# Optimization experiments

Hardware: AMD Instinct MI355X
Metric: run time of the kernel (lower is better)

The kernel has to match this reference:

```python
import jax, jax.numpy as jnp
import numpy as np

MODES, WIDTH, DEPTH, IN_F, OUT_F, HID = 8, 16, 3, 1, 1, 64


def setup_inputs() -> dict:
    key = jax.random.key(0)
    ks = jax.random.split(key, 12)
    B, H, W = 8, 512, 512
    scale = 1.0 / (WIDTH * WIDTH)
    inp = {
        'x': jax.random.normal(ks[0], (B, IN_F, H, W), dtype=jnp.float32),
        'fc0_w': jax.random.normal(ks[1], (IN_F, WIDTH), dtype=jnp.float32) * 0.5,
        'fc0_b': jax.random.normal(ks[2], (WIDTH,), dtype=jnp.float32) * 0.1,
        # complex spectral weights stored as real/imag parts, stacked over depth
        'spec_wr': jax.random.normal(ks[3], (DEPTH, WIDTH, WIDTH, MODES, MODES), dtype=jnp.float32) * scale,
        'spec_wi': jax.random.normal(ks[4], (DEPTH, WIDTH, WIDTH, MODES, MODES), dtype=jnp.float32) * scale,
        # 1x1 convs as [depth, out, in] matmuls + bias
        'conv_w': jax.random.normal(ks[5], (DEPTH, WIDTH, WIDTH), dtype=jnp.float32) * 0.25,
        'conv_b': jax.random.normal(ks[6], (DEPTH, WIDTH), dtype=jnp.float32) * 0.1,
        'fc1_w': jax.random.normal(ks[7], (WIDTH, HID), dtype=jnp.float32) * 0.25,
        'fc1_b': jax.random.normal(ks[8], (HID,), dtype=jnp.float32) * 0.1,
        'fc2_w': jax.random.normal(ks[9], (HID, OUT_F), dtype=jnp.float32) * 0.125,
        'fc2_b': jax.random.normal(ks[10], (OUT_F,), dtype=jnp.float32) * 0.1,
    }
    return inp


def _spectral_conv(x, w):
    # x: [B, Ci, H, W] real; w: [Ci, Co, m, m] complex
    B, C, H, W = x.shape
    m = w.shape[2]
    x_ft = jnp.fft.rfft2(x, norm='forward')  # [B, Ci, H, W//2+1]
    out_modes = jnp.einsum('bixy,ioxy->boxy', x_ft[:, :, :m, :m], w)
    out_ft = jnp.zeros((B, w.shape[1], H, W // 2 + 1), dtype=out_modes.dtype)
    out_ft = out_ft.at[:, :, :m, :m].set(out_modes)
    return jnp.fft.irfft2(out_ft, s=(H, W), norm='forward')


def reference(x, fc0_w, fc0_b, spec_wr, spec_wi, conv_w, conv_b, fc1_w, fc1_b, fc2_w, fc2_b):
    # lift: [B,C,H,W] -> channels-last linear -> [B,width,H,W]
    h = jnp.einsum('bchw,cd->bdhw', x, fc0_w) + fc0_b[None, :, None, None]
    for d in range(DEPTH):
        w_c = (spec_wr[d] + 1j * spec_wi[d]).astype(jnp.complex64)
        y = _spectral_conv(h, w_c)
        local = jnp.einsum('bchw,oc->bohw', h, conv_w[d]) + conv_b[d][None, :, None, None]
        h = y + local
    h = jnp.einsum('bchw,cd->bdhw', h, fc1_w) + fc1_b[None, :, None, None]
    h = jax.nn.relu(h)
    out = jnp.einsum('bchw,cd->bdhw', h, fc2_w) + fc2_b[None, :, None, None]
    return out
```

## Files before the change

### kernel.cpp

```cpp
#include <hip/hip_runtime.h>
#include <math.h>

#define NB 8
#define NH 512
#define NW 512
#define ANG512 0.01227184630308513f
#define SPEC_D 16384

typedef __attribute__((ext_vector_type(8))) _Float16 f16x8;
typedef __attribute__((ext_vector_type(4))) float    f32x4;

__global__ __launch_bounds__(256) void k_pre(const float* __restrict__ x,
                                             float* __restrict__ P) {
    __shared__ float wred[8][16];
    const int tid = threadIdx.x;
    const int w = tid >> 6, lane = tid & 63;
    const int gid = blockIdx.x;
    const int b = gid >> 6, rg = gid & 63;

    #pragma unroll
    for (int rr = 0; rr < 2; ++rr) {
        const int row = rg * 8 + w + 4 * rr;
        const float* xr = x + ((size_t)(b * NH + row)) * NW;

        float p[16];
        #pragma unroll
        for (int j = 0; j < 16; ++j) p[j] = 0.f;

        #pragma unroll
        for (int j = 0; j < 4; ++j) {
            const int ww = lane + (j << 6);
            const float xa = xr[ww], xb = xr[ww + 256];
            const float a = xa + xb, d = xa - xb;
            float c1, s1;
            __sincosf(ANG512 * (float)ww, &s1, &c1);
            p[0] += a;
            p[1] = fmaf(d, c1, p[1]);
            p[9] = fmaf(-d, s1, p[9]);
            const float c2k = 2.f * c1;
            float ckm = 1.f, skm = 0.f, ck = c1, sk = s1;
            #pragma unroll
            for (int k = 2; k < 8; ++k) {
                const float cn = fmaf(c2k, ck, -ckm);
                const float sn = fmaf(c2k, sk, -skm);
                ckm = ck; skm = sk; ck = cn; sk = sn;
                const float v = (k & 1) ? d : a;
                p[k]     = fmaf(v, ck, p[k]);
                p[8 + k] = fmaf(-v, sk, p[8 + k]);
            }
        }
        #pragma unroll
        for (int m = 1; m < 64; m <<= 1) {
            #pragma unroll
            for (int j = 0; j < 16; ++j) p[j] += __shfl_xor(p[j], m);
        }
        if (lane < 16) wred[w + 4 * rr][lane] = p[lane];
    }
    __syncthreads();

    if (tid < 128) {
        const int kx = tid >> 4, q = tid & 15, qm = q & 7;
        float acc = 0.f;
        #pragma unroll
        for (int r = 0; r < 8; ++r) {
            const int row = rg * 8 + r;
            const int m = (kx * row) & 511;
            float cm, s2;
            __sincosf(ANG512 * (float)m, &s2, &cm);
            const float rre = wred[r][qm], rim = wred[r][8 + qm];
            acc += (q < 8) ? (rre * cm + rim * s2)
                           : (rim * cm - rre * s2);
        }
        P[((size_t)((b * 64 + rg) * 8 + kx)) * 16 + q] = acc;
    }
}

__global__ __launch_bounds__(256) void k_modes(
        const float* __restrict__ P,
        const float* __restrict__ spec_wr, const float* __restrict__ spec_wi,
        const float* __restrict__ conv_w, const float* __restrict__ conv_b,
        const float* __restrict__ fc0_w, const float* __restrict__ fc0_b,
        const float* __restrict__ fc1_w, const float* __restrict__ fc1_b,
        float* __restrict__ AH, float* __restrict__ gv, float* __restrict__ Kv) {
    __shared__ __align__(16) float sm[2640];
    float* red2  = sm;
    float* X2    = sm + 256;
    float* Xr    = sm + 272;
    float* Xi    = sm + 400;
    float* Fr    = sm + 528;
    float* Fi    = sm + 656;
    float* Ar    = sm + 784;
    float* Ai    = sm + 912;
    float* Pm    = sm + 1040;
    float* fc1_s = sm + 1552;
    float* ps    = sm + 2576;

    const int tid = threadIdx.x;
    const int bid = blockIdx.x;
    const int b = bid >> 3;
    const int kx = bid & 7;

    {
        const int o = tid >> 4, c = tid & 15;
        float s = 0.f;
        for (int k = 0; k < 16; ++k)
            s += conv_w[512 + o * 16 + k] * conv_w[256 + k * 16 + c];
        Pm[tid] = s;
    }
    Pm[256 + tid] = conv_w[512 + tid];
    #pragma unroll
    for (int k = 0; k < 4; ++k) fc1_s[tid + k * 256] = fc1_w[tid + k * 256];

    {
        const int q = tid & 15, c = tid >> 4;
        float acc = 0.f;
        #pragma unroll
        for (int m = 0; m < 4; ++m) {
            const int rg = c + 16 * m;
            acc += P[((size_t)((b * 64 + rg) * 8 + kx)) * 16 + q];
        }
        red2[c * 16 + q] = acc;
    }
    __syncthreads();
    if (tid < 16) {
        float s = 0.f;
        #pragma unroll
        for (int c = 0; c < 16; ++c) s += red2[c * 16 + tid];
        X2[tid] = s;
    }
    __syncthreads();

    const bool act = (tid < 128);
    const int o = tid >> 3, ky = tid & 7;
    if (act) {
        const float inv = 1.f / (512.f * 512.f);
        float xr0 = fc0_w[o] * X2[ky] * inv;
        float xi0 = fc0_w[o] * X2[8 + ky] * inv;
        if (kx == 0 && ky == 0) xr0 += fc0_b[o];
        Xr[o * 8 + ky] = xr0; Xi[o * 8 + ky] = xi0;
        Ar[o * 8 + ky] = 0.f; Ai[o * 8 + ky] = 0.f;
    }
    __syncthreads();

    for (int dd = 0; dd < 3; ++dd) {
        if (act) {
            float fr = 0.f, fi = 0.f;
            const float* wrp = spec_wr + (size_t)dd * SPEC_D + o * 64 + kx * 8 + ky;
            const float* wip = spec_wi + (size_t)dd * SPEC_D + o * 64 + kx * 8 + ky;
            #pragma unroll
            for (int i = 0; i < 16; ++i) {
                const float wre = wrp[i * 1024];
                const float wim = wip[i * 1024];
                const float xr0 = Xr[i * 8 + ky], xi0 = Xi[i * 8 + ky];
                fr += xr0 * wre - xi0 * wim;
                fi += xr0 * wim + xi0 * wre;
            }
            Fr[o * 8 + ky] = fr; Fi[o * 8 + ky] = fi;
        }
        __syncthreads();
        float xnr = 0.f, xni = 0.f;
        if (act) {
            float ar, ai;
            if (dd == 2) {
                ar = Fr[o * 8 + ky]; ai = Fi[o * 8 + ky];
            } else {
                ar = 0.f; ai = 0.f;
                #pragma unroll
                for (int c = 0; c < 16; ++c) {
                    const float pv = Pm[dd * 256 + o * 16 + c];
                    ar = fmaf(pv, Fr[c * 8 + ky], ar);
                    ai = fmaf(pv, Fi[c * 8 + ky], ai);
                }
            }
            Ar[o * 8 + ky] += ar; Ai[o * 8 + ky] += ai;
            if (dd < 2) {
                const float fr0 = Fr[o * 8 + ky], fi0 = Fi[o * 8 + ky];
                if (ky == 0) {
                    if (kx == 0) { xnr = fr0; xni = 0.f; }
                    else         { xnr = 0.5f * fr0; xni = 0.5f * fi0; }
                } else { xnr = fr0; xni = fi0; }
                #pragma unroll
                for (int c = 0; c < 16; ++c) {
                    const float cc = conv_w[dd * 256 + o * 16 + c];
                    xnr = fmaf(cc, Xr[c * 8 + ky], xnr);
                    xni = fmaf(cc, Xi[c * 8 + ky], xni);
                }
                if (kx == 0 && ky == 0) xnr += conv_b[dd * 16 + o];
            }
        }
        __syncthreads();
        if (act && dd < 2) { Xr[o * 8 + ky] = xnr; Xi[o * 8 + ky] = xni; }
        __syncthreads();
    }

    #pragma unroll
    for (int k2 = 0; k2 < 2; ++k2) {
        const int idx = tid + k2 * 256;
        const int hd = idx >> 3, ky2 = idx & 7;
        float ar = 0.f, ai = 0.f;
        #pragma unroll
        for (int c = 0; c < 16; ++c) {
            const float f = fc1_s[c * 64 + hd];
            ar = fmaf(f, Ar[c * 8 + ky2], ar);
            ai = fmaf(f, Ai[c * 8 + ky2], ai);
        }
        const float ck = (ky2 == 0) ? 1.f : 2.f;
        const size_t off = ((((size_t)(b * 64 + hd)) * 8 + ky2) * 8 + kx) * 2;
        AH[off]     = ck * ar;
        AH[off + 1] = ck * ai;
    }

    if (kx == 0) {
        if (tid < 16) {
            float su = 0.f, sb = 0.f;
            for (int c = 0; c < 16; ++c) {
                su += conv_w[tid * 16 + c] * fc0_w[c];
                sb += conv_w[tid * 16 + c] * fc0_b[c];
            }
            ps[tid] = su; ps[16 + tid] = sb;
        }
        __syncthreads();
        if (tid < 16) {
            float dv = 0.f, ev = conv_b[32 + tid];
            for (int k = 0; k < 16; ++k) {
                dv += Pm[tid * 16 + k] * ps[k];
                ev += Pm[tid * 16 + k] * (ps[16 + k] + conv_b[k]);
                ev += conv_w[512 + tid * 16 + k] * conv_b[16 + k];
            }
            ps[32 + tid] = dv; ps[48 + tid] = ev;
        }
        __syncthreads();
        if (tid < 64) {
            float g = 0.f, K = fc1_b[tid];
            for (int c = 0; c < 16; ++c) {
                g = fmaf(fc1_w[c * 64 + tid], ps[32 + c], g);
                K = fmaf(fc1_w[c * 64 + tid], ps[48 + c], K);
            }
            gv[b * 64 + tid] = g;
            Kv[b * 64 + tid] = K;
        }
    }
}

__global__ __launch_bounds__(256, 4) void k_head(
        const float* __restrict__ x, const float* __restrict__ AH,
        const float* __restrict__ gv, const float* __restrict__ Kv,
        const float* __restrict__ fc2_w, const float* __restrict__ fc2_b,
        float* __restrict__ out) {
    __shared__ __align__(16) _Float16 Ef[2][512][8];
    __shared__ __align__(16) _Float16 Apk[4][4][64][8];

    const int tid  = threadIdx.x;
    const int lane = tid & 63;
    const int rl   = tid >> 6;
    const int b    = blockIdx.x >> 7;
    const int rp   = blockIdx.x & 127;
    const int row  = rp * 4 + rl;

    #pragma unroll
    for (int pxi = 0; pxi < 2; ++pxi) {
        const int px = tid + pxi * 256;
        float c1, s1;
        __sincosf(ANG512 * (float)px, &s1, &c1);
        float ck = 1.f, sk = 0.f;
        #pragma unroll
        for (int k = 0; k < 8; ++k) {
            Ef[0][px][k] = (_Float16)ck;
            Ef[1][px][k] = (_Float16)(-sk);
            const float cn = ck * c1 - sk * s1;
            const float sn = sk * c1 + ck * s1;
            ck = cn; sk = sn;
        }
    }

    float ghr[16], w2r[16];
    {
        const int lg = lane >> 4;
        #pragma unroll
        for (int t = 0; t < 4; ++t)
            #pragma unroll
            for (int v = 0; v < 4; ++v) {
                const int hd = t * 16 + lg * 4 + v;
                ghr[t * 4 + v] = gv[b * 64 + hd];
                w2r[t * 4 + v] = fc2_w[hd];
            }
    }

    {
        float c1, s1;
        __sincosf(ANG512 * (float)row, &s1, &c1);
        float ctr[8], str[8];
        ctr[0] = 1.f; str[0] = 0.f; ctr[1] = c1; str[1] = s1;
        const float c2k = 2.f * c1;
        #pragma unroll
        for (int k = 2; k < 8; ++k) {
            ctr[k] = fmaf(c2k, ctr[k - 1], -ctr[k - 2]);
            str[k] = fmaf(c2k, str[k - 1], -str[k - 2]);
        }
        #pragma unroll
        for (int j = 0; j < 8; ++j) {
            const int idx = lane + j * 64;
            const int hd = idx >> 3, ky = idx & 7;
            const float4* ap = (const float4*)(AH + ((size_t)(b * 64 + hd) * 8 + ky) * 16);
            const float4 a0 = ap[0], a1 = ap[1], a2 = ap[2], a3 = ap[3];
            float wr = a0.x, wi = a0.y;
            wr = fmaf(a0.z, ctr[1], wr); wr = fmaf(-a0.w, str[1], wr);
            wi = fmaf(a0.z, str[1], wi); wi = fmaf(a0.w, ctr[1], wi);
            wr = fmaf(a1.x, ctr[2], wr); wr = fmaf(-a1.y, str[2], wr);
            wi = fmaf(a1.x, str[2], wi); wi = fmaf(a1.y, ctr[2], wi);
            wr = fmaf(a1.z, ctr[3], wr); wr = fmaf(-a1.w, str[3], wr);
            wi = fmaf(a1.z, str[3], wi); wi = fmaf(a1.w, ctr[3], wi);
            wr = fmaf(a2.x, ctr[4], wr); wr = fmaf(-a2.y, str[4], wr);
            wi = fmaf(a2.x, str[4], wi); wi = fmaf(a2.y, ctr[4], wi);
            wr = fmaf(a2.z, ctr[5], wr); wr = fmaf(-a2.w, str[5], wr);
            wi = fmaf(a2.z, str[5], wi); wi = fmaf(a2.w, ctr[5], wi);
            wr = fmaf(a3.x, ctr[6], wr); wr = fmaf(-a3.y, str[6], wr);
            wi = fmaf(a3.x, str[6], wi); wi = fmaf(a3.y, ctr[6], wi);
            wr = fmaf(a3.z, ctr[7], wr); wr = fmaf(-a3.w, str[7], wr);
            wi = fmaf(a3.w, ctr[7], wi); wi = fmaf(a3.z, str[7], wi);
            if (ky == 0) wr += Kv[b * 64 + hd];
            const _Float16 hr  = (_Float16)wr;
            const _Float16 hi_ = (_Float16)wi;
            Apk[rl][0][hd][ky] = hr;
            Apk[rl][1][hd][ky] = hi_;
            Apk[rl][2][hd][ky] = (_Float16)(wr - (float)hr);
            Apk[rl][3][hd][ky] = (_Float16)(wi - (float)hi_);
        }
    }
    __syncthreads();

    f16x8 a1[4];
    {
        const int kb = lane >> 4, m = lane & 15;
        #pragma unroll
        for (int t = 0; t < 4; ++t)
            a1[t] = *(const f16x8*)&Apk[rl][kb][t * 16 + m][0];
    }

    const int eb = (lane >> 4) & 1, n = lane & 15;
    const float fc2b = fc2_b[0];
    const float* xrow = x + ((size_t)(b * NH + row)) * NW;
    float* orow = out + ((size_t)(b * NH + row)) * NW;

    f16x8 bn0 = *(const f16x8*)&Ef[eb][n][0];
    f16x8 bn1 = *(const f16x8*)&Ef[eb][16 + n][0];
    float xn0 = xrow[n];
    float xn1 = xrow[16 + n];

    #pragma unroll 2
    for (int it = 0; it < 16; ++it) {
        const f16x8 b0 = bn0, b1 = bn1;
        const float x0 = xn0, x1 = xn1;
        if (it < 15) {
            const int pb = (it + 1) * 32 + n;
            bn0 = *(const f16x8*)&Ef[eb][pb][0];
            bn1 = *(const f16x8*)&Ef[eb][pb + 16][0];
            xn0 = xrow[pb];
            xn1 = xrow[pb + 16];
        }
        f32x4 c0[4], c1[4];
        #pragma unroll
        for (int t = 0; t < 4; ++t) {
            c0[t] = (f32x4){0.f, 0.f, 0.f, 0.f};
            c1[t] = (f32x4){0.f, 0.f, 0.f, 0.f};
            c0[t] = __builtin_amdgcn_mfma_f32_16x16x32_f16(a1[t], b0, c0[t], 0, 0, 0);
            c1[t] = __builtin_amdgcn_mfma_f32_16x16x32_f16(a1[t], b1, c1[t], 0, 0, 0);
        }
        float p0[4] = {0.f, 0.f, 0.f, 0.f};
        float p1[4] = {0.f, 0.f, 0.f, 0.f};
        #pragma unroll
        for (int t = 0; t < 4; ++t)
            #pragma unroll
            for (int v = 0; v < 4; ++v) {
                float s0 = fmaf(ghr[t * 4 + v], x0, c0[t][v]);
                float s1 = fmaf(ghr[t * 4 + v], x1, c1[t][v]);
                s0 = fmaxf(s0, 0.f);
                s1 = fmaxf(s1, 0.f);
                p0[v] = fmaf(s0, w2r[t * 4 + v], p0[v]);
                p1[v] = fmaf(s1, w2r[t * 4 + v], p1[v]);
            }
        float v0 = (p0[0] + p0[1]) + (p0[2] + p0[3]);
        float v1 = (p1[0] + p1[1]) + (p1[2] + p1[3]);
        v0 += __shfl_xor(v0, 16);
        v1 += __shfl_xor(v1, 16);
        v0 += __shfl_xor(v0, 32);
        v1 += __shfl_xor(v1, 32);
        if (lane < 16) {
            orow[it * 32 + lane]      = v0 + fc2b;
            orow[it * 32 + 16 + lane] = v1 + fc2b;
        }
    }
}

extern "C" void kernel_launch(void* const* d_in, const int* in_sizes, int n_in,
                              void* d_out, int out_size, void* d_ws, size_t ws_size,
                              hipStream_t stream) {
    const float* x       = (const float*)d_in[0];
    const float* fc0_w   = (const float*)d_in[1];
    const float* fc0_b   = (const float*)d_in[2];
    const float* spec_wr = (const float*)d_in[3];
    const float* spec_wi = (const float*)d_in[4];
    const float* conv_w  = (const float*)d_in[5];
    const float* conv_b  = (const float*)d_in[6];
    const float* fc1_w   = (const float*)d_in[7];
    const float* fc1_b   = (const float*)d_in[8];
    const float* fc2_w   = (const float*)d_in[9];
    const float* fc2_b   = (const float*)d_in[10];
    float* outp = (float*)d_out;

    char* ws = (char*)d_ws;
    float* P  = (float*)ws;
    float* AH = (float*)(ws + 262144);
    float* gv = (float*)(ws + 524288);
    float* Kv = (float*)(ws + 526336);

    k_pre<<<512, 256, 0, stream>>>(x, P);
    k_modes<<<64, 256, 0, stream>>>(P, spec_wr, spec_wi, conv_w, conv_b,
                                    fc0_w, fc0_b, fc1_w, fc1_b, AH, gv, Kv);
    k_head<<<1024, 256, 0, stream>>>(x, AH, gv, Kv, fc2_w, fc2_b, outp);
}
```

Before: 116.2 us.

## Fuse modes kernel into head kernel with per-batch flag synchronization

Merges the small 64-block mode-mixing kernel into the 1024-block head kernel. The first 64 blocks do the mode work, publish AH/gv/Kv with atomic stores and raise a per-batch release flag. Every block builds its twiddle tables first, then spins on its batch's flag before reading those values. This removes one kernel launch and its serialization gap, and lets the head's table setup overlap the mode computation. In exchange it relies on the producer blocks being scheduled (deadlock risk if they are not resident), uses only relaxed loads on the consumer side, and adds spin-wait overhead.

```diff
diff --git a/kernel.cpp b/kernel.cpp
--- a/kernel.cpp
+++ b/kernel.cpp
@@ -7,8 +7,13 @@
 #define ANG512 0.01227184630308513f
 #define SPEC_D 16384
 
+#define DEV_SCOPE __HIP_MEMORY_SCOPE_AGENT
+
 typedef __attribute__((ext_vector_type(8))) _Float16 f16x8;
 typedef __attribute__((ext_vector_type(4))) float    f32x4;
+
+__device__ int g_flag[256];
+__device__ int g_done[256];
 
 __global__ __launch_bounds__(256) void k_pre(const float* __restrict__ x,
                                              float* __restrict__ P) {
@@ -75,177 +80,14 @@
     }
 }
 
-__global__ __launch_bounds__(256) void k_modes(
-        const float* __restrict__ P,
+__global__ __launch_bounds__(256, 4) void k_mh(
+        const float* __restrict__ x, const float* __restrict__ P,
         const float* __restrict__ spec_wr, const float* __restrict__ spec_wi,
         const float* __restrict__ conv_w, const float* __restrict__ conv_b,
         const float* __restrict__ fc0_w, const float* __restrict__ fc0_b,
         const float* __restrict__ fc1_w, const float* __restrict__ fc1_b,
-        float* __restrict__ AH, float* __restrict__ gv, float* __restrict__ Kv) {
-    __shared__ __align__(16) float sm[2640];
-    float* red2  = sm;
-    float* X2    = sm + 256;
-    float* Xr    = sm + 272;
-    float* Xi    = sm + 400;
-    float* Fr    = sm + 528;
-    float* Fi    = sm + 656;
-    float* Ar    = sm + 784;
-    float* Ai    = sm + 912;
-    float* Pm    = sm + 1040;
-    float* fc1_s = sm + 1552;
-    float* ps    = sm + 2576;
-
-    const int tid = threadIdx.x;
-    const int bid = blockIdx.x;
-    const int b = bid >> 3;
-    const int kx = bid & 7;
-
-    {
-        const int o = tid >> 4, c = tid & 15;
-        float s = 0.f;
-        for (int k = 0; k < 16; ++k)
-            s += conv_w[512 + o * 16 + k] * conv_w[256 + k * 16 + c];
-        Pm[tid] = s;
-    }
-    Pm[256 + tid] = conv_w[512 + tid];
-    #pragma unroll
-    for (int k = 0; k < 4; ++k) fc1_s[tid + k * 256] = fc1_w[tid + k * 256];
-
-    {
-        const int q = tid & 15, c = tid >> 4;
-        float acc = 0.f;
-        #pragma unroll
-        for (int m = 0; m < 4; ++m) {
-            const int rg = c + 16 * m;
-            acc += P[((size_t)((b * 64 + rg) * 8 + kx)) * 16 + q];
-        }
-        red2[c * 16 + q] = acc;
-    }
-    __syncthreads();
-    if (tid < 16) {
-        float s = 0.f;
-        #pragma unroll
-        for (int c = 0; c < 16; ++c) s += red2[c * 16 + tid];
-        X2[tid] = s;
-    }
-    __syncthreads();
-
-    const bool act = (tid < 128);
-    const int o = tid >> 3, ky = tid & 7;
-    if (act) {
-        const float inv = 1.f / (512.f * 512.f);
-        float xr0 = fc0_w[o] * X2[ky] * inv;
-        float xi0 = fc0_w[o] * X2[8 + ky] * inv;
-        if (kx == 0 && ky == 0) xr0 += fc0_b[o];
-        Xr[o * 8 + ky] = xr0; Xi[o * 8 + ky] = xi0;
-        Ar[o * 8 + ky] = 0.f; Ai[o * 8 + ky] = 0.f;
-    }
-    __syncthreads();
-
-    for (int dd = 0; dd < 3; ++dd) {
-        if (act) {
-            float fr = 0.f, fi = 0.f;
-            const float* wrp = spec_wr + (size_t)dd * SPEC_D + o * 64 + kx * 8 + ky;
-            const float* wip = spec_wi + (size_t)dd * SPEC_D + o * 64 + kx * 8 + ky;
-            #pragma unroll
-            for (int i = 0; i < 16; ++i) {
-                const float wre = wrp[i * 1024];
-                const float wim = wip[i * 1024];
-                const float xr0 = Xr[i * 8 + ky], xi0 = Xi[i * 8 + ky];
-                fr += xr0 * wre - xi0 * wim;
-                fi += xr0 * wim + xi0 * wre;
-            }
-            Fr[o * 8 + ky] = fr; Fi[o * 8 + ky] = fi;
-        }
-        __syncthreads();
-        float xnr = 0.f, xni = 0.f;
-        if (act) {
-            float ar, ai;
-            if (dd == 2) {
-                ar = Fr[o * 8 + ky]; ai = Fi[o * 8 + ky];
-            } else {
-                ar = 0.f; ai = 0.f;
-                #pragma unroll
-                for (int c = 0; c < 16; ++c) {
-                    const float pv = Pm[dd * 256 + o * 16 + c];
-                    ar = fmaf(pv, Fr[c * 8 + ky], ar);
-                    ai = fmaf(pv, Fi[c * 8 + ky], ai);
-                }
-            }
-            Ar[o * 8 + ky] += ar; Ai[o * 8 + ky] += ai;
-            if (dd < 2) {
-                const float fr0 = Fr[o * 8 + ky], fi0 = Fi[o * 8 + ky];
-                if (ky == 0) {
-                    if (kx == 0) { xnr = fr0; xni = 0.f; }
-                    else         { xnr = 0.5f * fr0; xni = 0.5f * fi0; }
-                } else { xnr = fr0; xni = fi0; }
-                #pragma unroll
-                for (int c = 0; c < 16; ++c) {
-                    const float cc = conv_w[dd * 256 + o * 16 + c];
-                    xnr = fmaf(cc, Xr[c * 8 + ky], xnr);
-                    xni = fmaf(cc, Xi[c * 8 + ky], xni);
-                }
-                if (kx == 0 && ky == 0) xnr += conv_b[dd * 16 + o];
-            }
-        }
-        __syncthreads();
-        if (act && dd < 2) { Xr[o * 8 + ky] = xnr; Xi[o * 8 + ky] = xni; }
-        __syncthreads();
-    }
-
-    #pragma unroll
-    for (int k2 = 0; k2 < 2; ++k2) {
-        const int idx = tid + k2 * 256;
-        const int hd = idx >> 3, ky2 = idx & 7;
-        float ar = 0.f, ai = 0.f;
-        #pragma unroll
-        for (int c = 0; c < 16; ++c) {
-            const float f = fc1_s[c * 64 + hd];
-            ar = fmaf(f, Ar[c * 8 + ky2], ar);
-            ai = fmaf(f, Ai[c * 8 + ky2], ai);
-        }
-        const float ck = (ky2 == 0) ? 1.f : 2.f;
-        const size_t off = ((((size_t)(b * 64 + hd)) * 8 + ky2) * 8 + kx) * 2;
-        AH[off]     = ck * ar;
-        AH[off + 1] = ck * ai;
-    }
-
-    if (kx == 0) {
-        if (tid < 16) {
-            float su = 0.f, sb = 0.f;
-            for (int c = 0; c < 16; ++c) {
-                su += conv_w[tid * 16 + c] * fc0_w[c];
-                sb += conv_w[tid * 16 + c] * fc0_b[c];
-            }
-            ps[tid] = su; ps[16 + tid] = sb;
-        }
-        __syncthreads();
-        if (tid < 16) {
-            float dv = 0.f, ev = conv_b[32 + tid];
-            for (int k = 0; k < 16; ++k) {
-                dv += Pm[tid * 16 + k] * ps[k];
-                ev += Pm[tid * 16 + k] * (ps[16 + k] + conv_b[k]);
-                ev += conv_w[512 + tid * 16 + k] * conv_b[16 + k];
-            }
-            ps[32 + tid] = dv; ps[48 + tid] = ev;
-        }
-        __syncthreads();
-        if (tid < 64) {
-            float g = 0.f, K = fc1_b[tid];
-            for (int c = 0; c < 16; ++c) {
-                g = fmaf(fc1_w[c * 64 + tid], ps[32 + c], g);
-                K = fmaf(fc1_w[c * 64 + tid], ps[48 + c], K);
-            }
-            gv[b * 64 + tid] = g;
-            Kv[b * 64 + tid] = K;
-        }
-    }
-}
-
-__global__ __launch_bounds__(256, 4) void k_head(
-        const float* __restrict__ x, const float* __restrict__ AH,
-        const float* __restrict__ gv, const float* __restrict__ Kv,
         const float* __restrict__ fc2_w, const float* __restrict__ fc2_b,
+        float* __restrict__ AH, float* __restrict__ gv, float* __restrict__ Kv,
         float* __restrict__ out) {
     __shared__ __align__(16) _Float16 Ef[2][512][8];
     __shared__ __align__(16) _Float16 Apk[4][4][64][8];
@@ -253,9 +95,172 @@
     const int tid  = threadIdx.x;
     const int lane = tid & 63;
     const int rl   = tid >> 6;
-    const int b    = blockIdx.x >> 7;
-    const int rp   = blockIdx.x & 127;
+    const int bid  = blockIdx.x;
+    const int cb   = bid >> 7;
+    const int rp   = bid & 127;
     const int row  = rp * 4 + rl;
+
+    if (bid < 64) {
+        float* psm   = (float*)&Apk[0][0][0][0];
+        float* red2  = psm;
+        float* X2    = psm + 256;
+        float* Xr    = psm + 272;
+        float* Xi    = psm + 400;
+        float* Fr    = psm + 528;
+        float* Fi    = psm + 656;
+        float* Ar    = psm + 784;
+        float* Ai    = psm + 912;
+        float* Pm    = psm + 1040;
+        float* fc1_s = psm + 1552;
+        float* ps    = psm + 2576;
+
+        const int b2 = bid >> 3;
+        const int kx = bid & 7;
+
+        {
+            const int o = tid >> 4, c = tid & 15;
+            float s = 0.f;
+            for (int k = 0; k < 16; ++k)
+                s += conv_w[512 + o * 16 + k] * conv_w[256 + k * 16 + c];
+            Pm[tid] = s;
+        }
+        Pm[256 + tid] = conv_w[512 + tid];
+        #pragma unroll
+        for (int k = 0; k < 4; ++k) fc1_s[tid + k * 256] = fc1_w[tid + k * 256];
+
+        {
+            const int q = tid & 15, c = tid >> 4;
+            float acc = 0.f;
+            #pragma unroll
+            for (int m = 0; m < 4; ++m) {
+                const int rg = c + 16 * m;
+                acc += P[((size_t)((b2 * 64 + rg) * 8 + kx)) * 16 + q];
+            }
+            red2[c * 16 + q] = acc;
+        }
+        __syncthreads();
+        if (tid < 16) {
+            float s = 0.f;
+            #pragma unroll
+            for (int c = 0; c < 16; ++c) s += red2[c * 16 + tid];
+            X2[tid] = s;
+        }
+        __syncthreads();
+
+        const bool act = (tid < 128);
+        const int o = tid >> 3, ky = tid & 7;
+        if (act) {
+            const float inv = 1.f / (512.f * 512.f);
+            float xr0 = fc0_w[o] * X2[ky] * inv;
+            float xi0 = fc0_w[o] * X2[8 + ky] * inv;
+            if (kx == 0 && ky == 0) xr0 += fc0_b[o];
+            Xr[o * 8 + ky] = xr0; Xi[o * 8 + ky] = xi0;
+            Ar[o * 8 + ky] = 0.f; Ai[o * 8 + ky] = 0.f;
+        }
+        __syncthreads();
+
+        for (int dd = 0; dd < 3; ++dd) {
+            if (act) {
+                float fr = 0.f, fi = 0.f;
+                const float* wrp = spec_wr + (size_t)dd * SPEC_D + o * 64 + kx * 8 + ky;
+                const float* wip = spec_wi + (size_t)dd * SPEC_D + o * 64 + kx * 8 + ky;
+                #pragma unroll
+                for (int i = 0; i < 16; ++i) {
+                    const float wre = wrp[i * 1024];
+                    const float wim = wip[i * 1024];
+                    const float xr0 = Xr[i * 8 + ky], xi0 = Xi[i * 8 + ky];
+                    fr += xr0 * wre - xi0 * wim;
+                    fi += xr0 * wim + xi0 * wre;
+                }
+                Fr[o * 8 + ky] = fr; Fi[o * 8 + ky] = fi;
+            }
+            __syncthreads();
+            float xnr = 0.f, xni = 0.f;
+            if (act) {
+                float ar, ai;
+                if (dd == 2) {
+                    ar = Fr[o * 8 + ky]; ai = Fi[o * 8 + ky];
+                } else {
+                    ar = 0.f; ai = 0.f;
+                    #pragma unroll
+                    for (int c = 0; c < 16; ++c) {
+                        const float pv = Pm[dd * 256 + o * 16 + c];
+                        ar = fmaf(pv, Fr[c * 8 + ky], ar);
+                        ai = fmaf(pv, Fi[c * 8 + ky], ai);
+                    }
+                }
+                Ar[o * 8 + ky] += ar; Ai[o * 8 + ky] += ai;
+                if (dd < 2) {
+                    const float fr0 = Fr[o * 8 + ky], fi0 = Fi[o * 8 + ky];
+                    if (ky == 0) {
+                        if (kx == 0) { xnr = fr0; xni = 0.f; }
+                        else         { xnr = 0.5f * fr0; xni = 0.5f * fi0; }
+                    } else { xnr = fr0; xni = fi0; }
+                    #pragma unroll
+                    for (int c = 0; c < 16; ++c) {
+                        const float cc = conv_w[dd * 256 + o * 16 + c];
+                        xnr = fmaf(cc, Xr[c * 8 + ky], xnr);
+                        xni = fmaf(cc, Xi[c * 8 + ky], xni);
+                    }
+                    if (kx == 0 && ky == 0) xnr += conv_b[dd * 16 + o];
+                }
+            }
+            __syncthreads();
+            if (act && dd < 2) { Xr[o * 8 + ky] = xnr; Xi[o * 8 + ky] = xni; }
+            __syncthreads();
+        }
+
+        #pragma unroll
+        for (int k2 = 0; k2 < 2; ++k2) {
+            const int idx = tid + k2 * 256;
+            const int hd = idx >> 3, ky2 = idx & 7;
+            float ar = 0.f, ai = 0.f;
+            #pragma unroll
+            for (int c = 0; c < 16; ++c) {
+                const float f = fc1_s[c * 64 + hd];
+                ar = fmaf(f, Ar[c * 8 + ky2], ar);
+                ai = fmaf(f, Ai[c * 8 + ky2], ai);
+            }
+            const float ck = (ky2 == 0) ? 1.f : 2.f;
+            const size_t off = ((((size_t)(b2 * 64 + hd)) * 8 + ky2) * 8 + kx) * 2;
+            __hip_atomic_store(&AH[off],     ck * ar, __ATOMIC_RELAXED, DEV_SCOPE);
+            __hip_atomic_store(&AH[off + 1], ck * ai, __ATOMIC_RELAXED, DEV_SCOPE);
+        }
+
+        if (kx == 0) {
+            if (tid < 16) {
+                float su = 0.f, sb = 0.f;
+                for (int c = 0; c < 16; ++c) {
+                    su += conv_w[tid * 16 + c] * fc0_w[c];
+                    sb += conv_w[tid * 16 + c] * fc0_b[c];
+                }
+                ps[tid] = su; ps[16 + tid] = sb;
+            }
+            __syncthreads();
+            if (tid < 16) {
+                float dv = 0.f, ev = conv_b[32 + tid];
+                for (int k = 0; k < 16; ++k) {
+                    dv += Pm[tid * 16 + k] * ps[k];
+                    ev += Pm[tid * 16 + k] * (ps[16 + k] + conv_b[k]);
+                    ev += conv_w[512 + tid * 16 + k] * conv_b[16 + k];
+                }
+                ps[32 + tid] = dv; ps[48 + tid] = ev;
+            }
+            __syncthreads();
+            if (tid < 64) {
+                float g = 0.f, K = fc1_b[tid];
+                for (int c = 0; c < 16; ++c) {
+                    g = fmaf(fc1_w[c * 64 + tid], ps[32 + c], g);
+                    K = fmaf(fc1_w[c * 64 + tid], ps[48 + c], K);
+                }
+                __hip_atomic_store(&gv[b2 * 64 + tid], g, __ATOMIC_RELAXED, DEV_SCOPE);
+                __hip_atomic_store(&Kv[b2 * 64 + tid], K, __ATOMIC_RELAXED, DEV_SCOPE);
+            }
+        }
+        __syncthreads();
+        if (tid == 0)
+            __hip_atomic_fetch_add(&g_flag[b2 * 32], 1, __ATOMIC_RELEASE, DEV_SCOPE);
+    }
 
     #pragma unroll
     for (int pxi = 0; pxi < 2; ++pxi) {
@@ -273,6 +278,18 @@
         }
     }
 
+    if (tid == 0) {
+        while (__hip_atomic_load(&g_flag[cb * 32], __ATOMIC_RELAXED, DEV_SCOPE) < 8)
+            __builtin_amdgcn_s_sleep(4);
+        const int d = __hip_atomic_fetch_add(&g_done[cb * 32], 1,
+                                             __ATOMIC_RELAXED, DEV_SCOPE);
+        if (d == 127) {
+            __hip_atomic_store(&g_flag[cb * 32], 0, __ATOMIC_RELAXED, DEV_SCOPE);
+            __hip_atomic_store(&g_done[cb * 32], 0, __ATOMIC_RELAXED, DEV_SCOPE);
+        }
+    }
+    __syncthreads();
+
     float ghr[16], w2r[16];
     {
         const int lg = lane >> 4;
@@ -281,7 +298,7 @@
             #pragma unroll
             for (int v = 0; v < 4; ++v) {
                 const int hd = t * 16 + lg * 4 + v;
-                ghr[t * 4 + v] = gv[b * 64 + hd];
+                ghr[t * 4 + v] = gv[cb * 64 + hd];
                 w2r[t * 4 + v] = fc2_w[hd];
             }
     }
@@ -301,7 +318,7 @@
         for (int j = 0; j < 8; ++j) {
             const int idx = lane + j * 64;
             const int hd = idx >> 3, ky = idx & 7;
-            const float4* ap = (const float4*)(AH + ((size_t)(b * 64 + hd) * 8 + ky) * 16);
+            const float4* ap = (const float4*)(AH + ((size_t)(cb * 64 + hd) * 8 + ky) * 16);
             const float4 a0 = ap[0], a1 = ap[1], a2 = ap[2], a3 = ap[3];
             float wr = a0.x, wi = a0.y;
             wr = fmaf(a0.z, ctr[1], wr); wr = fmaf(-a0.w, str[1], wr);
@@ -318,7 +335,7 @@
             wi = fmaf(a3.x, str[6], wi); wi = fmaf(a3.y, ctr[6], wi);
             wr = fmaf(a3.z, ctr[7], wr); wr = fmaf(-a3.w, str[7], wr);
             wi = fmaf(a3.w, ctr[7], wi); wi = fmaf(a3.z, str[7], wi);
-            if (ky == 0) wr += Kv[b * 64 + hd];
+            if (ky == 0) wr += Kv[cb * 64 + hd];
             const _Float16 hr  = (_Float16)wr;
             const _Float16 hi_ = (_Float16)wi;
             Apk[rl][0][hd][ky] = hr;
@@ -339,8 +356,8 @@
 
     const int eb = (lane >> 4) & 1, n = lane & 15;
     const float fc2b = fc2_b[0];
-    const float* xrow = x + ((size_t)(b * NH + row)) * NW;
-    float* orow = out + ((size_t)(b * NH + row)) * NW;
+    const float* xrow = x + ((size_t)(cb * NH + row)) * NW;
+    float* orow = out + ((size_t)(cb * NH + row)) * NW;
 
     f16x8 bn0 = *(const f16x8*)&Ef[eb][n][0];
     f16x8 bn1 = *(const f16x8*)&Ef[eb][16 + n][0];
@@ -415,7 +432,7 @@
     float* Kv = (float*)(ws + 526336);
 
     k_pre<<<512, 256, 0, stream>>>(x, P);
-    k_modes<<<64, 256, 0, stream>>>(P, spec_wr, spec_wi, conv_w, conv_b,
-                                    fc0_w, fc0_b, fc1_w, fc1_b, AH, gv, Kv);
-    k_head<<<1024, 256, 0, stream>>>(x, AH, gv, Kv, fc2_w, fc2_b, outp);
+    k_mh<<<1024, 256, 0, stream>>>(x, P, spec_wr, spec_wi, conv_w, conv_b,
+                                   fc0_w, fc0_b, fc1_w, fc1_b, fc2_w, fc2_b,
+                                   AH, gv, Kv, outp);
 }
```

New measurement: 119.3 us. +2.6%, slower.

## Split k_head work across more blocks with two waves per row

Applied to the files above, without the earlier changes.

Each k_head block now covers two rows and half the columns instead of four full rows. Two waves share one row: they split the AH twiddle packing work and each handles a quarter of the columns. This gives four times as many blocks, a smaller LDS footprint and a higher occupancy target, aimed at better latency hiding and load balance across CUs. In exchange, the sincos tables and the per-row AH packing are recomputed by more blocks, adding redundant setup work per output.

```diff
diff --git a/kernel.cpp b/kernel.cpp
--- a/kernel.cpp
+++ b/kernel.cpp
@@ -242,31 +242,35 @@
     }
 }
 
-__global__ __launch_bounds__(256, 4) void k_head(
+__global__ __launch_bounds__(256, 8) void k_head(
         const float* __restrict__ x, const float* __restrict__ AH,
         const float* __restrict__ gv, const float* __restrict__ Kv,
         const float* __restrict__ fc2_w, const float* __restrict__ fc2_b,
         float* __restrict__ out) {
-    __shared__ __align__(16) _Float16 Ef[2][512][8];
-    __shared__ __align__(16) _Float16 Apk[4][4][64][8];
+    __shared__ __align__(16) _Float16 Ef[2][256][8];
+    __shared__ __align__(16) _Float16 Apk[2][4][64][8];
 
     const int tid  = threadIdx.x;
     const int lane = tid & 63;
-    const int rl   = tid >> 6;
-    const int b    = blockIdx.x >> 7;
-    const int rp   = blockIdx.x & 127;
-    const int row  = rp * 4 + rl;
-
-    #pragma unroll
-    for (int pxi = 0; pxi < 2; ++pxi) {
-        const int px = tid + pxi * 256;
+    const int wid  = tid >> 6;
+    const int rl   = wid >> 1;
+    const int jh   = wid & 1;
+    const int bid  = blockIdx.x;
+    const int b    = bid >> 9;
+    const int rem  = bid & 511;
+    const int rpp  = rem >> 1;
+    const int h    = rem & 1;
+    const int row  = rpp * 2 + rl;
+
+    {
+        const int pxg = h * 256 + tid;
         float c1, s1;
-        __sincosf(ANG512 * (float)px, &s1, &c1);
+        __sincosf(ANG512 * (float)pxg, &s1, &c1);
         float ck = 1.f, sk = 0.f;
         #pragma unroll
         for (int k = 0; k < 8; ++k) {
-            Ef[0][px][k] = (_Float16)ck;
-            Ef[1][px][k] = (_Float16)(-sk);
+            Ef[0][tid][k] = (_Float16)ck;
+            Ef[1][tid][k] = (_Float16)(-sk);
             const float cn = ck * c1 - sk * s1;
             const float sn = sk * c1 + ck * s1;
             ck = cn; sk = sn;
@@ -298,8 +302,8 @@
             str[k] = fmaf(c2k, str[k - 1], -str[k - 2]);
         }
         #pragma unroll
-        for (int j = 0; j < 8; ++j) {
-            const int idx = lane + j * 64;
+        for (int j = 0; j < 4; ++j) {
+            const int idx = lane + (jh * 4 + j) * 64;
             const int hd = idx >> 3, ky = idx & 7;
             const float4* ap = (const float4*)(AH + ((size_t)(b * 64 + hd) * 8 + ky) * 16);
             const float4 a0 = ap[0], a1 = ap[1], a2 = ap[2], a3 = ap[3];
@@ -341,22 +345,25 @@
     const float fc2b = fc2_b[0];
     const float* xrow = x + ((size_t)(b * NH + row)) * NW;
     float* orow = out + ((size_t)(b * NH + row)) * NW;
-
-    f16x8 bn0 = *(const f16x8*)&Ef[eb][n][0];
-    f16x8 bn1 = *(const f16x8*)&Ef[eb][16 + n][0];
-    float xn0 = xrow[n];
-    float xn1 = xrow[16 + n];
-
-    #pragma unroll 2
-    for (int it = 0; it < 16; ++it) {
+    const int tb = jh * 8;
+    const int gb = h * 16 + tb;
+
+    f16x8 bn0 = *(const f16x8*)&Ef[eb][tb * 16 + n][0];
+    f16x8 bn1 = *(const f16x8*)&Ef[eb][(tb + 1) * 16 + n][0];
+    float xn0 = xrow[gb * 16 + n];
+    float xn1 = xrow[(gb + 1) * 16 + n];
+
+    #pragma unroll
+    for (int it = 0; it < 4; ++it) {
         const f16x8 b0 = bn0, b1 = bn1;
         const float x0 = xn0, x1 = xn1;
-        if (it < 15) {
-            const int pb = (it + 1) * 32 + n;
-            bn0 = *(const f16x8*)&Ef[eb][pb][0];
-            bn1 = *(const f16x8*)&Ef[eb][pb + 16][0];
-            xn0 = xrow[pb];
-            xn1 = xrow[pb + 16];
+        if (it < 3) {
+            const int tl = tb + 2 * (it + 1);
+            const int gl = gb + 2 * (it + 1);
+            bn0 = *(const f16x8*)&Ef[eb][tl * 16 + n][0];
+            bn1 = *(const f16x8*)&Ef[eb][(tl + 1) * 16 + n][0];
+            xn0 = xrow[gl * 16 + n];
+            xn1 = xrow[(gl + 1) * 16 + n];
         }
         f32x4 c0[4], c1[4];
         #pragma unroll
@@ -386,8 +393,9 @@
         v0 += __shfl_xor(v0, 32);
         v1 += __shfl_xor(v1, 32);
         if (lane < 16) {
-            orow[it * 32 + lane]      = v0 + fc2b;
-            orow[it * 32 + 16 + lane] = v1 + fc2b;
+            const int g0 = gb + 2 * it;
+            orow[g0 * 16 + lane]        = v0 + fc2b;
+            orow[(g0 + 1) * 16 + lane]  = v1 + fc2b;
         }
     }
 }
@@ -417,5 +425,5 @@
     k_pre<<<512, 256, 0, stream>>>(x, P);
     k_modes<<<64, 256, 0, stream>>>(P, spec_wr, spec_wi, conv_w, conv_b,
                                     fc0_w, fc0_b, fc1_w, fc1_b, AH, gv, Kv);
-    k_head<<<1024, 256, 0, stream>>>(x, AH, gv, Kv, fc2_w, fc2_b, outp);
+    k_head<<<4096, 256, 0, stream>>>(x, AH, gv, Kv, fc2_w, fc2_b, outp);
 }
```

After: 217.4 us. 87.1% more time.
